# Optimization experiments

Hardware: AMD Instinct MI355X
Metric: run time of the kernel (lower is better)

The kernel has to match this reference:

```python
import jax, jax.numpy as jnp
import numpy as np

B, S, E, HEADS, LATENT = 8, 4096, 2048, 16, 64
HEAD_SIZE = E // HEADS  # 128
NEG = -1e20


def setup_inputs() -> dict:
    key = jax.random.key(0)
    k0, k1, k2, k3, k4 = jax.random.split(key, 5)
    return {
        "x": jax.random.normal(k0, (B, S, E), dtype=jnp.float32) * 0.02,
        "W_dkv": jax.random.normal(k1, (LATENT, E), dtype=jnp.float32) * 0.02,
        "W_k": jax.random.normal(k2, (HEAD_SIZE, LATENT), dtype=jnp.float32) * 0.02,
        "W_v": jax.random.normal(k3, (HEAD_SIZE, LATENT), dtype=jnp.float32) * 0.02,
        "W_q": jax.random.normal(k4, (HEAD_SIZE, E), dtype=jnp.float32) * 0.02,
    }


def reference(x, W_dkv, W_k, W_v, W_q):
    # x: [B,S,E]; nn.Linear computes x @ W.T (weight layout [out,in])
    head_size = W_k.shape[0]
    latent = jnp.einsum("bse,le->bsl", x, W_dkv)        # latent KV cache [B,S,L]
    absorbed_q = W_q.T @ W_k                              # [E,H] @ [H,L] -> [E,L]
    q_res = jnp.einsum("bse,el->bsl", x, absorbed_q)     # [B,S,L]
    scale = head_size ** -0.5
    scores = jnp.einsum("bql,bkl->bqk", q_res, latent) * scale  # [B,S,S]
    seq = x.shape[1]
    causal = jnp.tril(jnp.ones((seq, seq), dtype=bool))
    scores = jnp.where(causal, scores, NEG)
    attn = jax.nn.softmax(scores, axis=-1)               # dropout skipped (eval mode)
    v = jnp.einsum("bsl,hl->bsh", latent, W_v)           # compressed V [B,S,H]
    out = jnp.einsum("bqk,bkh->bqh", attn, v)            # [B,S,head_size]
    return out, latent  # latent == kv_cache returned by the module
```

## Files before the change

kernel.cpp:

```cpp
#include <hip/hip_runtime.h>
#include <hip/hip_bf16.h>

#define NB 8
#define NS 4096
#define NE 2048
#define NL 64
#define NH 128
#define NM (NB*NS)

typedef unsigned short ushort_t;
typedef __attribute__((ext_vector_type(4))) float f32x4;
typedef __attribute__((ext_vector_type(8))) __bf16 bf16x8;
typedef __attribute__((ext_vector_type(8))) unsigned short u16x8;
typedef __attribute__((ext_vector_type(4))) unsigned short u16x4;

#define SCALE2 0.1275174537f

__device__ __forceinline__ float fast_exp2(float x) {
    return __builtin_amdgcn_exp2f(x);
}

__device__ __forceinline__ unsigned short f2bf(float f) {
    union { float f; unsigned u; } v; v.f = f;
    unsigned u = v.u + 0x7fffu + ((v.u >> 16) & 1u);
    return (unsigned short)(u >> 16);
}

__device__ __forceinline__ float bf2f(ushort_t u) {
    union { unsigned u; float f; } v; v.u = (unsigned)u << 16; return v.f;
}

__device__ __forceinline__ int swz(int row, int colbyte) {
    return (row * 128 + colbyte) ^ ((row & 7) << 4);
}

__device__ __forceinline__ void wg_barrier() {
    asm volatile("s_waitcnt lgkmcnt(0)" ::: "memory");
    __builtin_amdgcn_s_barrier();
    __builtin_amdgcn_sched_barrier(0);
}

__global__ __launch_bounds__(256) void prep_kernel(
    const float* __restrict__ Wdkv, const float* __restrict__ Wk,
    const float* __restrict__ Wq, ushort_t* __restrict__ WcatT)
{
    __shared__ float wk[128 * 64];
    const int t = threadIdx.x;
    for (int i = t; i < 128 * 64; i += 256) wk[i] = Wk[i];
    __syncthreads();
    const int e = blockIdx.x * 256 + t;
    const int l0 = blockIdx.y * 16;
    float acc[16];
    #pragma unroll
    for (int l = 0; l < 16; ++l) acc[l] = 0.f;
    for (int h = 0; h < 128; ++h) {
        float q = Wq[h * NE + e];
        #pragma unroll
        for (int l = 0; l < 16; ++l) acc[l] += q * wk[h * 64 + l0 + l];
    }
    for (int l = 0; l < 16; ++l) WcatT[(64 + l0 + l) * NE + e] = f2bf(acc[l] * SCALE2);
    for (int l = 0; l < 16; ++l) WcatT[(l0 + l) * NE + e] = f2bf(Wdkv[(l0 + l) * NE + e]);
}

__global__ __launch_bounds__(256) void proj_kernel(
    const float* __restrict__ x, const ushort_t* __restrict__ WcatT,
    float* __restrict__ latent_out, ushort_t* __restrict__ k_bf,
    ushort_t* __restrict__ q_bf, ushort_t* __restrict__ kt)
{
    __shared__ ushort_t As[2][64 * 64];
    __shared__ ushort_t Bs[2][128 * 64];
    const int tid = threadIdx.x;
    const int w = tid >> 6, lane = tid & 63, lg = lane >> 4, li = lane & 15;
    const int m0 = blockIdx.x * 64;
    const int wm = (w >> 1) * 32, wn = (w & 1) * 64;
    const int srow = tid >> 3, scol = tid & 7;

    f32x4 acc[2][4];
    #pragma unroll
    for (int i = 0; i < 2; ++i)
        #pragma unroll
        for (int j = 0; j < 4; ++j) acc[i][j] = f32x4{0.f, 0.f, 0.f, 0.f};

    f32x4 a0reg[2][2], a1reg[2][2];
    u16x8 b0reg[4], b1reg[4];

#define PLOAD(k0, AR, BR) do { \
    _Pragma("unroll") for (int p = 0; p < 2; ++p) { \
        const float* gp = x + (long)(m0 + srow + 32 * p) * NE + (k0) + scol * 8; \
        AR[p][0] = *reinterpret_cast<const f32x4*>(gp); \
        AR[p][1] = *reinterpret_cast<const f32x4*>(gp + 4); } \
    _Pragma("unroll") for (int p = 0; p < 4; ++p) \
        BR[p] = *reinterpret_cast<const u16x8*>(WcatT + (long)(srow + 32 * p) * NE + (k0) + scol * 8); \
} while (0)

#define PWRITE(AR, BR, buf) do { \
    _Pragma("unroll") for (int p = 0; p < 2; ++p) { \
        union { unsigned uw[4]; u16x8 v; } hu; \
        asm("v_cvt_pk_bf16_f32 %0, %1, %2" : "=v"(hu.uw[0]) : "v"(AR[p][0][0]), "v"(AR[p][0][1])); \
        asm("v_cvt_pk_bf16_f32 %0, %1, %2" : "=v"(hu.uw[1]) : "v"(AR[p][0][2]), "v"(AR[p][0][3])); \
        asm("v_cvt_pk_bf16_f32 %0, %1, %2" : "=v"(hu.uw[2]) : "v"(AR[p][1][0]), "v"(AR[p][1][1])); \
        asm("v_cvt_pk_bf16_f32 %0, %1, %2" : "=v"(hu.uw[3]) : "v"(AR[p][1][2]), "v"(AR[p][1][3])); \
        *reinterpret_cast<u16x8*>(reinterpret_cast<char*>(As[buf]) + swz(srow + 32 * p, scol * 16)) = hu.v; } \
    _Pragma("unroll") for (int p = 0; p < 4; ++p) \
        *reinterpret_cast<u16x8*>(reinterpret_cast<char*>(Bs[buf]) + swz(srow + 32 * p, scol * 16)) = BR[p]; \
} while (0)

    auto compute = [&](int buf) {
        #pragma unroll
        for (int c = 0; c < 2; ++c) {
            bf16x8 af[2], bfv[4];
            #pragma unroll
            for (int mf = 0; mf < 2; ++mf)
                af[mf] = *reinterpret_cast<const bf16x8*>(
                    reinterpret_cast<const char*>(As[buf]) + swz(wm + 16 * mf + li, c * 64 + lg * 16));
            #pragma unroll
            for (int nf = 0; nf < 4; ++nf)
                bfv[nf] = *reinterpret_cast<const bf16x8*>(
                    reinterpret_cast<const char*>(Bs[buf]) + swz(wn + 16 * nf + li, c * 64 + lg * 16));
            #pragma unroll
            for (int mf = 0; mf < 2; ++mf)
                #pragma unroll
                for (int nf = 0; nf < 4; ++nf)
                    acc[mf][nf] = __builtin_amdgcn_mfma_f32_16x16x32_bf16(
                        af[mf], bfv[nf], acc[mf][nf], 0, 0, 0);
        }
    };

    PLOAD(0, a0reg, b0reg);
    PLOAD(64, a1reg, b1reg);
    PWRITE(a0reg, b0reg, 0);
    wg_barrier();

    for (int ks = 0; ks < 32; ks += 2) {
        if (ks + 2 < 32) PLOAD((ks + 2) * 64, a0reg, b0reg);
        compute(0);
        PWRITE(a1reg, b1reg, 1);
        wg_barrier();
        if (ks + 3 < 32) PLOAD((ks + 3) * 64, a1reg, b1reg);
        compute(1);
        if (ks + 2 < 32) PWRITE(a0reg, b0reg, 0);
        wg_barrier();
    }

    const int b = m0 >> 12, s0 = m0 & 4095;
    #pragma unroll
    for (int mf = 0; mf < 2; ++mf) {
        #pragma unroll
        for (int nf = 0; nf < 4; ++nf) {
            int col = wn + 16 * nf + li;
            #pragma unroll
            for (int r = 0; r < 4; ++r) {
                int row = m0 + wm + 16 * mf + 4 * lg + r;
                float v = acc[mf][nf][r];
                if (wn == 0) {
                    latent_out[(long)row * NL + col] = v;
                    k_bf[(long)row * NL + col] = f2bf(v);
                    *reinterpret_cast<ushort_t*>(reinterpret_cast<char*>(As[0]) +
                        swz(wm + 16 * mf + 4 * lg + r, col * 2)) = f2bf(v);
                } else {
                    q_bf[(long)row * NL + (col - 64)] = f2bf(v);
                }
            }
        }
    }
    wg_barrier();
    union { u16x8 u; bf16x8 v; } iu;
    #pragma unroll
    for (int j = 0; j < 8; ++j)
        iu.u[j] = (lg == (li >> 3) + 2 * (w & 1) && (li & 7) == j)
                      ? (ushort_t)0x3F80 : (ushort_t)0;
    const int ckt = w >> 1;
    f32x4 ktacc[4];
    #pragma unroll
    for (int nf = 0; nf < 4; ++nf) {
        bf16x8 bfv = *reinterpret_cast<const bf16x8*>(
            reinterpret_cast<const char*>(As[0]) + swz(16 * nf + li, ckt * 64 + lg * 16));
        ktacc[nf] = __builtin_amdgcn_mfma_f32_16x16x32_bf16(
            iu.v, bfv, f32x4{0.f, 0.f, 0.f, 0.f}, 0, 0, 0);
    }
    #pragma unroll
    for (int nf = 0; nf < 4; ++nf)
        #pragma unroll
        for (int r = 0; r < 4; ++r)
            kt[(long)(b * 64 + 16 * w + 4 * lg + r) * NS + s0 + 16 * nf + li] =
                f2bf(ktacc[nf][r]);
}

__global__ __launch_bounds__(256, 2) void attn_kernel(
    const ushort_t* __restrict__ q_bf, const ushort_t* __restrict__ k_bf,
    const ushort_t* __restrict__ kt, const float* __restrict__ Wv,
    float* __restrict__ out)
{
    __shared__ __attribute__((aligned(16))) char smem[65536];
    ushort_t* OW = (ushort_t*)smem;
    float* mw = (float*)(smem + 32768);
    float* lw = (float*)(smem + 33792);
    ushort_t* Ms = (ushort_t*)(smem + 36864);
    ushort_t* Wvs = (ushort_t*)(smem + 45056);
    float* Os = (float*)smem;

    const int tid = threadIdx.x;
    const int w = tid >> 6, lane = tid & 63, lg = lane >> 4, li = lane & 15;
    const int l = blockIdx.x;
    const int b = l & 7;
    const int p_ = l >> 3;
    const int k_ = p_ >> 1, e_ = p_ & 1, kk = (k_ & 15) * 2;
    const int qt = (k_ >> 4) ? (e_ ? kk + 1 : 63 - kk) : (e_ ? 62 - kk : kk);
    const int Q0 = qt << 6;
    const int nch = (qt >> 1) + 1;

    const int krow = tid >> 1, khalf = tid & 1;
    const int trow = tid >> 2, tkq = (tid & 3) * 32;

    bf16x8 qf[4][2];
    #pragma unroll
    for (int qb = 0; qb < 4; ++qb)
        #pragma unroll
        for (int c = 0; c < 2; ++c)
            qf[qb][c] = *reinterpret_cast<const bf16x8*>(
                q_bf + ((long)b * NS + Q0 + 16 * qb + li) * NL + c * 32 + lg * 8);

    float m_r[4], l_r[4];
    #pragma unroll
    for (int qb = 0; qb < 4; ++qb) { m_r[qb] = -1.0e30f; l_r[qb] = 0.f; }
    f32x4 oacc[4][4];
    #pragma unroll
    for (int qb = 0; qb < 4; ++qb)
        #pragma unroll
        for (int n = 0; n < 4; ++n) oacc[qb][n] = f32x4{0.f, 0.f, 0.f, 0.f};

    u16x8 k0reg[4], t0reg[4], k1reg[4], t1reg[4];

#define ALOAD(ch, KR, TR) do { \
    const int kv0_ = (ch) * 128; \
    _Pragma("unroll") for (int pp = 0; pp < 4; ++pp) \
        KR[pp] = *reinterpret_cast<const u16x8*>( \
            k_bf + ((long)b * NS + kv0_ + krow) * NL + khalf * 32 + pp * 8); \
    _Pragma("unroll") for (int pp = 0; pp < 4; ++pp) \
        TR[pp] = *reinterpret_cast<const u16x8*>( \
            kt + ((long)b * 64 + trow) * NS + kv0_ + tkq + pp * 8); \
} while (0)

#define AWRITE(KR, TR, buf) do { \
    char* Kb_ = smem + (buf) * 16384; \
    char* Tb_ = smem + 32768 + (buf) * 16384; \
    _Pragma("unroll") for (int pp = 0; pp < 4; ++pp) \
        *reinterpret_cast<u16x8*>(Kb_ + swz(krow, khalf * 64 + pp * 16)) = KR[pp]; \
    _Pragma("unroll") for (int pp = 0; pp < 4; ++pp) { \
        const int kv8 = tkq + pp * 8; \
        const int colp = (kv8 & 0x60) | ((kv8 & 0xC) << 1) | ((kv8 & 0x10) >> 2); \
        const int xo = (trow & 15) << 4; \
        u16x4 lo = {TR[pp][0], TR[pp][1], TR[pp][2], TR[pp][3]}; \
        u16x4 hi = {TR[pp][4], TR[pp][5], TR[pp][6], TR[pp][7]}; \
        *reinterpret_cast<u16x4*>(Tb_ + trow * 256 + ((colp * 2) ^ xo)) = lo; \
        *reinterpret_cast<u16x4*>(Tb_ + trow * 256 + (((colp + 8) * 2) ^ xo)) = hi; \
    } \
} while (0)

    auto compute = [&](int buf, bool diag, int kv0) {
        const char* Kb = smem + buf * 16384;
        const char* Tb = smem + 32768 + buf * 16384;
        f32x4 s[2][4];
        #pragma unroll
        for (int kvb = 0; kvb < 2; ++kvb)
            #pragma unroll
            for (int qb = 0; qb < 4; ++qb) s[kvb][qb] = f32x4{0.f, 0.f, 0.f, 0.f};
        __builtin_amdgcn_s_setprio(1);
        #pragma unroll
        for (int c = 0; c < 2; ++c)
            #pragma unroll
            for (int kvb = 0; kvb < 2; ++kvb) {
                bf16x8 a = *reinterpret_cast<const bf16x8*>(
                    Kb + swz(32 * w + 16 * kvb + li, c * 64 + lg * 16));
                #pragma unroll
                for (int qb = 0; qb < 4; ++qb)
                    s[kvb][qb] = __builtin_amdgcn_mfma_f32_16x16x32_bf16(
                        a, qf[qb][c], s[kvb][qb], 0, 0, 0);
            }
        __builtin_amdgcn_s_setprio(0);
        if (diag) {
            #pragma unroll
            for (int kvb = 0; kvb < 2; ++kvb)
                #pragma unroll
                for (int qb = 0; qb < 4; ++qb)
                    #pragma unroll
                    for (int r = 0; r < 4; ++r) {
                        int kv_g = kv0 + 32 * w + 16 * kvb + 4 * lg + r;
                        int q_g = Q0 + 16 * qb + li;
                        if (kv_g > q_g) s[kvb][qb][r] = -3.0e38f;
                    }
        }
        float mx[4];
        #pragma unroll
        for (int qb = 0; qb < 4; ++qb) {
            float m0_ = fmaxf(fmaxf(s[0][qb][0], s[0][qb][1]), fmaxf(s[0][qb][2], s[0][qb][3]));
            float m1_ = fmaxf(fmaxf(s[1][qb][0], s[1][qb][1]), fmaxf(s[1][qb][2], s[1][qb][3]));
            mx[qb] = fmaxf(m0_, m1_);
        }
        bool ok = (mx[0] <= m_r[0] + 8.f) && (mx[1] <= m_r[1] + 8.f) &&
                  (mx[2] <= m_r[2] + 8.f) && (mx[3] <= m_r[3] + 8.f);
        if (!__all(ok)) {
            #pragma unroll
            for (int qb = 0; qb < 4; ++qb) {
                float mxf = fmaxf(mx[qb], __shfl_xor(mx[qb], 16));
                mxf = fmaxf(mxf, __shfl_xor(mxf, 32));
                float m_new = fmaxf(m_r[qb], mxf);
                float corr = fast_exp2(m_r[qb] - m_new);
                m_r[qb] = m_new;
                l_r[qb] *= corr;
                float corrO[4];
                #pragma unroll
                for (int r = 0; r < 4; ++r)
                    corrO[r] = __shfl(corr, (lane & 48) | (4 * lg + r));
                #pragma unroll
                for (int n = 0; n < 4; ++n)
                    #pragma unroll
                    for (int r = 0; r < 4; ++r) oacc[qb][n][r] *= corrO[r];
            }
        }
        #pragma unroll
        for (int qb = 0; qb < 4; ++qb) {
            float rs = 0.f;
            #pragma unroll
            for (int kvb = 0; kvb < 2; ++kvb)
                #pragma unroll
                for (int r = 0; r < 4; ++r) {
                    float pv = fast_exp2(s[kvb][qb][r] - m_r[qb]);
                    s[kvb][qb][r] = pv;
                    rs += pv;
                }
            l_r[qb] += rs;
        }
        bf16x8 vb[4];
        #pragma unroll
        for (int n = 0; n < 4; ++n)
            vb[n] = *reinterpret_cast<const bf16x8*>(
                Tb + (16 * n + li) * 256 + ((64 * w + 16 * lg) ^ (li << 4)));
        __builtin_amdgcn_s_setprio(1);
        #pragma unroll
        for (int qb = 0; qb < 4; ++qb) {
            union { unsigned uw[4]; bf16x8 v; } pa;
            asm("v_cvt_pk_bf16_f32 %0, %1, %2" : "=v"(pa.uw[0]) : "v"(s[0][qb][0]), "v"(s[0][qb][1]));
            asm("v_cvt_pk_bf16_f32 %0, %1, %2" : "=v"(pa.uw[1]) : "v"(s[0][qb][2]), "v"(s[0][qb][3]));
            asm("v_cvt_pk_bf16_f32 %0, %1, %2" : "=v"(pa.uw[2]) : "v"(s[1][qb][0]), "v"(s[1][qb][1]));
            asm("v_cvt_pk_bf16_f32 %0, %1, %2" : "=v"(pa.uw[3]) : "v"(s[1][qb][2]), "v"(s[1][qb][3]));
            #pragma unroll
            for (int n = 0; n < 4; ++n)
                oacc[qb][n] = __builtin_amdgcn_mfma_f32_16x16x32_bf16(
                    pa.v, vb[n], oacc[qb][n], 0, 0, 0);
        }
        __builtin_amdgcn_s_setprio(0);
    };

    ALOAD(0, k0reg, t0reg);
    if (nch >= 2) ALOAD(1, k1reg, t1reg);
    AWRITE(k0reg, t0reg, 0);
    wg_barrier();
    for (int i = 0; i < nch; i += 2) {
        if (i + 2 < nch) ALOAD(i + 2, k0reg, t0reg);
        compute(0, i == nch - 1, i * 128);
        if (i + 1 < nch) AWRITE(k1reg, t1reg, 1);
        wg_barrier();
        if (i + 1 >= nch) break;
        if (i + 3 < nch) ALOAD(i + 3, k1reg, t1reg);
        compute(1, i + 1 == nch - 1, (i + 1) * 128);
        if (i + 2 < nch) AWRITE(k0reg, t0reg, 0);
        wg_barrier();
    }

    #pragma unroll
    for (int qb = 0; qb < 4; ++qb) {
        l_r[qb] += __shfl_xor(l_r[qb], 16);
        l_r[qb] += __shfl_xor(l_r[qb], 32);
    }
    if (lg == 0) {
        #pragma unroll
        for (int qb = 0; qb < 4; ++qb) {
            mw[w * 64 + 16 * qb + li] = m_r[qb];
            lw[w * 64 + 16 * qb + li] = l_r[qb];
        }
    }
    #pragma unroll
    for (int qb = 0; qb < 4; ++qb)
        #pragma unroll
        for (int r = 0; r < 4; ++r) {
            union { unsigned uw[2]; u16x4 v; } u;
            asm("v_cvt_pk_bf16_f32 %0, %1, %2" : "=v"(u.uw[0]) : "v"(oacc[qb][0][r]), "v"(oacc[qb][1][r]));
            asm("v_cvt_pk_bf16_f32 %0, %1, %2" : "=v"(u.uw[1]) : "v"(oacc[qb][2][r]), "v"(oacc[qb][3][r]));
            int q = 16 * qb + 4 * lg + r;
            *reinterpret_cast<u16x4*>(OW + (w * 64 + q) * 64 + li * 4) = u.v;
        }
    wg_barrier();

    {
        const int q = tid >> 2, g = tid & 3;
        float m4[4], l4[4];
        #pragma unroll
        for (int ww = 0; ww < 4; ++ww) { m4[ww] = mw[ww * 64 + q]; l4[ww] = lw[ww * 64 + q]; }
        float M = fmaxf(fmaxf(m4[0], m4[1]), fmaxf(m4[2], m4[3]));
        float cw[4], L = 0.f;
        #pragma unroll
        for (int ww = 0; ww < 4; ++ww) { cw[ww] = fast_exp2(m4[ww] - M); L += cw[ww] * l4[ww]; }
        float inv = 1.f / L;
        float merged[16];
        #pragma unroll
        for (int e = 0; e < 16; ++e) {
            float a = 0.f;
            #pragma unroll
            for (int ww = 0; ww < 4; ++ww)
                a += cw[ww] * bf2f(OW[(ww * 64 + q) * 64 + e * 4 + g]);
            merged[e] = a * inv;
        }
        #pragma unroll
        for (int ee = 0; ee < 8; ++ee) {
            unsigned pk;
            asm("v_cvt_pk_bf16_f32 %0, %1, %2" : "=v"(pk) : "v"(merged[2 * ee]), "v"(merged[2 * ee + 1]));
            *reinterpret_cast<unsigned*>(reinterpret_cast<char*>(Ms) + swz(q, g * 32 + 4 * ee)) = pk;
        }
        const int r = tid >> 1, hf = tid & 1;
        const float* wp = Wv + r * 64 + hf * 32;
        #pragma unroll
        for (int qq = 0; qq < 2; ++qq) {
            f32x4 w0 = *reinterpret_cast<const f32x4*>(wp + qq * 16);
            f32x4 w1 = *reinterpret_cast<const f32x4*>(wp + qq * 16 + 4);
            f32x4 w2 = *reinterpret_cast<const f32x4*>(wp + qq * 16 + 8);
            f32x4 w3 = *reinterpret_cast<const f32x4*>(wp + qq * 16 + 12);
            u16x8 h0, h1;
            #pragma unroll
            for (int jj = 0; jj < 4; ++jj) {
                h0[jj] = f2bf(w0[jj]); h0[4 + jj] = f2bf(w1[jj]);
                h1[jj] = f2bf(w2[jj]); h1[4 + jj] = f2bf(w3[jj]);
            }
            *reinterpret_cast<u16x8*>(reinterpret_cast<char*>(Wvs) + swz(r, hf * 64 + qq * 32)) = h0;
            *reinterpret_cast<u16x8*>(reinterpret_cast<char*>(Wvs) + swz(r, hf * 64 + qq * 32 + 16)) = h1;
        }
    }
    wg_barrier();

    f32x4 vacc[2][4];
    #pragma unroll
    for (int i = 0; i < 2; ++i)
        #pragma unroll
        for (int j = 0; j < 4; ++j) vacc[i][j] = f32x4{0.f, 0.f, 0.f, 0.f};
    #pragma unroll
    for (int c = 0; c < 2; ++c) {
        bf16x8 af[2], bfv[4];
        #pragma unroll
        for (int mf = 0; mf < 2; ++mf)
            af[mf] = *reinterpret_cast<const bf16x8*>(
                reinterpret_cast<const char*>(Wvs) + swz(32 * w + 16 * mf + li, c * 64 + lg * 16));
        #pragma unroll
        for (int nf = 0; nf < 4; ++nf)
            bfv[nf] = *reinterpret_cast<const bf16x8*>(
                reinterpret_cast<const char*>(Ms) + swz(16 * nf + li, c * 64 + lg * 16));
        #pragma unroll
        for (int mf = 0; mf < 2; ++mf)
            #pragma unroll
            for (int nf = 0; nf < 4; ++nf)
                vacc[mf][nf] = __builtin_amdgcn_mfma_f32_16x16x32_bf16(
                    af[mf], bfv[nf], vacc[mf][nf], 0, 0, 0);
    }
    wg_barrier();
    #pragma unroll
    for (int mf = 0; mf < 2; ++mf)
        #pragma unroll
        for (int nf = 0; nf < 4; ++nf)
            #pragma unroll
            for (int r = 0; r < 4; ++r)
                Os[(16 * nf + li) * 132 + 32 * w + 16 * mf + 4 * lg + r] = vacc[mf][nf][r];
    wg_barrier();
    {
        const int r = tid >> 2, cb = (tid & 3) * 32;
        float* op = out + ((long)b * NS + Q0 + r) * NH + cb;
        const float* sp = Os + r * 132 + cb;
        #pragma unroll
        for (int qq = 0; qq < 8; ++qq)
            *reinterpret_cast<f32x4*>(op + 4 * qq) = *reinterpret_cast<const f32x4*>(sp + 4 * qq);
    }
}

extern "C" void kernel_launch(void* const* d_in, const int* in_sizes, int n_in,
                              void* d_out, int out_size, void* d_ws, size_t ws_size,
                              hipStream_t stream) {
    const float* x    = (const float*)d_in[0];
    const float* Wdkv = (const float*)d_in[1];
    const float* Wk   = (const float*)d_in[2];
    const float* Wv   = (const float*)d_in[3];
    const float* Wq   = (const float*)d_in[4];

    float* out = (float*)d_out;
    float* latent_out = out + (long)NM * NH;

    ushort_t* WcatT = (ushort_t*)d_ws;
    ushort_t* q_bf  = WcatT + 128 * NE;
    ushort_t* k_bf  = q_bf + (long)NM * NL;
    ushort_t* kt    = k_bf + (long)NM * NL;

    hipLaunchKernelGGL(prep_kernel, dim3(NE / 256, 4), dim3(256), 0, stream, Wdkv, Wk, Wq, WcatT);
    hipLaunchKernelGGL(proj_kernel, dim3(NM / 64), dim3(256), 0, stream,
                       x, WcatT, latent_out, k_bf, q_bf, kt);
    hipLaunchKernelGGL(attn_kernel, dim3(512), dim3(256), 0, stream,
                       q_bf, k_bf, kt, Wv, out);
}
```

Baseline: 133.4 us.

## Single-buffer attention LDS tiles to raise occupancy to four blocks per CU

Replaces the double-buffered K/K^T shared-memory staging with a single buffer and shrinks LDS from 64KB to 34KB. Launch bounds go from 2 to 4 blocks per CU, and the merge scratch (Ms, Wvs) is overlaid on the freed tile region, with an extra barrier so the merge reads finish before the overwrite. The aim is more resident waves to hide latency. In exchange each chunk now needs two barriers, load/compute overlap within a block drops to one chunk ahead, and the tighter register budget may cause spills.

```diff
diff --git a/kernel.cpp b/kernel.cpp
--- a/kernel.cpp
+++ b/kernel.cpp
@@ -186,17 +186,17 @@
                 f2bf(ktacc[nf][r]);
 }
 
-__global__ __launch_bounds__(256, 2) void attn_kernel(
+__global__ __launch_bounds__(256, 4) void attn_kernel(
     const ushort_t* __restrict__ q_bf, const ushort_t* __restrict__ k_bf,
     const ushort_t* __restrict__ kt, const float* __restrict__ Wv,
     float* __restrict__ out)
 {
-    __shared__ __attribute__((aligned(16))) char smem[65536];
+    __shared__ __attribute__((aligned(16))) char smem[34816];
     ushort_t* OW = (ushort_t*)smem;
     float* mw = (float*)(smem + 32768);
     float* lw = (float*)(smem + 33792);
-    ushort_t* Ms = (ushort_t*)(smem + 36864);
-    ushort_t* Wvs = (ushort_t*)(smem + 45056);
+    ushort_t* Ms = (ushort_t*)smem;
+    ushort_t* Wvs = (ushort_t*)(smem + 8192);
     float* Os = (float*)smem;
 
     const int tid = threadIdx.x;
@@ -229,37 +229,37 @@
         #pragma unroll
         for (int n = 0; n < 4; ++n) oacc[qb][n] = f32x4{0.f, 0.f, 0.f, 0.f};
 
-    u16x8 k0reg[4], t0reg[4], k1reg[4], t1reg[4];
-
-#define ALOAD(ch, KR, TR) do { \
+    u16x8 kreg[4], treg[4];
+
+#define ALOAD(ch) do { \
     const int kv0_ = (ch) * 128; \
     _Pragma("unroll") for (int pp = 0; pp < 4; ++pp) \
-        KR[pp] = *reinterpret_cast<const u16x8*>( \
+        kreg[pp] = *reinterpret_cast<const u16x8*>( \
             k_bf + ((long)b * NS + kv0_ + krow) * NL + khalf * 32 + pp * 8); \
     _Pragma("unroll") for (int pp = 0; pp < 4; ++pp) \
-        TR[pp] = *reinterpret_cast<const u16x8*>( \
+        treg[pp] = *reinterpret_cast<const u16x8*>( \
             kt + ((long)b * 64 + trow) * NS + kv0_ + tkq + pp * 8); \
 } while (0)
 
-#define AWRITE(KR, TR, buf) do { \
-    char* Kb_ = smem + (buf) * 16384; \
-    char* Tb_ = smem + 32768 + (buf) * 16384; \
+#define AWRITE() do { \
+    char* Kb_ = smem; \
+    char* Tb_ = smem + 16384; \
     _Pragma("unroll") for (int pp = 0; pp < 4; ++pp) \
-        *reinterpret_cast<u16x8*>(Kb_ + swz(krow, khalf * 64 + pp * 16)) = KR[pp]; \
+        *reinterpret_cast<u16x8*>(Kb_ + swz(krow, khalf * 64 + pp * 16)) = kreg[pp]; \
     _Pragma("unroll") for (int pp = 0; pp < 4; ++pp) { \
         const int kv8 = tkq + pp * 8; \
         const int colp = (kv8 & 0x60) | ((kv8 & 0xC) << 1) | ((kv8 & 0x10) >> 2); \
         const int xo = (trow & 15) << 4; \
-        u16x4 lo = {TR[pp][0], TR[pp][1], TR[pp][2], TR[pp][3]}; \
-        u16x4 hi = {TR[pp][4], TR[pp][5], TR[pp][6], TR[pp][7]}; \
+        u16x4 lo = {treg[pp][0], treg[pp][1], treg[pp][2], treg[pp][3]}; \
+        u16x4 hi = {treg[pp][4], treg[pp][5], treg[pp][6], treg[pp][7]}; \
         *reinterpret_cast<u16x4*>(Tb_ + trow * 256 + ((colp * 2) ^ xo)) = lo; \
         *reinterpret_cast<u16x4*>(Tb_ + trow * 256 + (((colp + 8) * 2) ^ xo)) = hi; \
     } \
 } while (0)
 
-    auto compute = [&](int buf, bool diag, int kv0) {
-        const char* Kb = smem + buf * 16384;
-        const char* Tb = smem + 32768 + buf * 16384;
+    auto compute = [&](bool diag, int kv0) {
+        const char* Kb = smem;
+        const char* Tb = smem + 16384;
         f32x4 s[2][4];
         #pragma unroll
         for (int kvb = 0; kvb < 2; ++kvb)
@@ -352,20 +352,17 @@
         __builtin_amdgcn_s_setprio(0);
     };
 
-    ALOAD(0, k0reg, t0reg);
-    if (nch >= 2) ALOAD(1, k1reg, t1reg);
-    AWRITE(k0reg, t0reg, 0);
-    wg_barrier();
-    for (int i = 0; i < nch; i += 2) {
-        if (i + 2 < nch) ALOAD(i + 2, k0reg, t0reg);
-        compute(0, i == nch - 1, i * 128);
-        if (i + 1 < nch) AWRITE(k1reg, t1reg, 1);
+    ALOAD(0);
+    AWRITE();
+    wg_barrier();
+    for (int i = 0; i < nch; ++i) {
+        if (i + 1 < nch) ALOAD(i + 1);
+        compute(i == nch - 1, i * 128);
         wg_barrier();
-        if (i + 1 >= nch) break;
-        if (i + 3 < nch) ALOAD(i + 3, k1reg, t1reg);
-        compute(1, i + 1 == nch - 1, (i + 1) * 128);
-        if (i + 2 < nch) AWRITE(k0reg, t0reg, 0);
-        wg_barrier();
+        if (i + 1 < nch) {
+            AWRITE();
+            wg_barrier();
+        }
     }
 
     #pragma unroll
@@ -392,6 +389,7 @@
         }
     wg_barrier();
 
+    float merged[16];
     {
         const int q = tid >> 2, g = tid & 3;
         float m4[4], l4[4];
@@ -402,7 +400,6 @@
         #pragma unroll
         for (int ww = 0; ww < 4; ++ww) { cw[ww] = fast_exp2(m4[ww] - M); L += cw[ww] * l4[ww]; }
         float inv = 1.f / L;
-        float merged[16];
         #pragma unroll
         for (int e = 0; e < 16; ++e) {
             float a = 0.f;
@@ -411,6 +408,11 @@
                 a += cw[ww] * bf2f(OW[(ww * 64 + q) * 64 + e * 4 + g]);
             merged[e] = a * inv;
         }
+    }
+    wg_barrier();
+
+    {
+        const int q = tid >> 2, g = tid & 3;
         #pragma unroll
         for (int ee = 0; ee < 8; ++ee) {
             unsigned pk;
```

Result: slower. 339.9 us (+154.8%).
